# Kernel tuning notes

Hardware: AMD Instinct MI355X
Metric: run time of the kernel (lower is better)

## Reference

```python
import jax, jax.numpy as jnp
import numpy as np
import math

T, B, D, H, DH, DI, V, L = 1024, 4, 512, 8, 64, 2048, 256, 8
STAGES = (2, 4, 2)   # pre, shortened, post layer counts (model_config)
SF = 4               # fixed boundary every SF tokens
S = T // SF          # number of segments


def setup_inputs() -> dict:
    key = jax.random.key(0)
    ks = jax.random.split(key, 12)
    sd = 0.02
    data = jax.random.randint(ks[0], (T, B), 0, V, dtype=jnp.int32)
    t = jnp.arange(T)
    boundaries_gt = jnp.tile(((t % SF) == (SF - 1)).astype(jnp.int32)[:, None], (1, B))
    return {
        'data': data,
        'boundaries_gt': boundaries_gt,
        'word_emb': jax.random.normal(ks[1], (V, D)) * sd,
        'r_w_bias': jax.random.normal(ks[2], (H, DH)) * sd,
        'r_r_bias': jax.random.normal(ks[3], (H, DH)) * sd,
        'null_group': jax.random.normal(ks[4], (1, 1, D)),
        'down_ln_g': jnp.ones((D,), jnp.float32),
        'down_ln_b': jnp.zeros((D,), jnp.float32),
        'qkv_w': jax.random.normal(ks[5], (L, 3 * H * DH, D)) * sd,
        'rk_w': jax.random.normal(ks[6], (L, H * DH, D)) * sd,
        'o_w': jax.random.normal(ks[7], (L, D, H * DH)) * sd,
        'ln1_g': jnp.ones((L, D), jnp.float32),
        'ln1_b': jnp.zeros((L, D), jnp.float32),
        'ff_w1': jax.random.normal(ks[8], (L, DI, D)) * sd,
        'ff_b1': jnp.zeros((L, DI), jnp.float32),
        'ff_w2': jax.random.normal(ks[9], (L, D, DI)) * sd,
        'ff_b2': jnp.zeros((L, D), jnp.float32),
        'ln2_g': jnp.ones((L, D), jnp.float32),
        'ln2_b': jnp.zeros((L, D), jnp.float32),
        'final_w': jax.random.normal(ks[10], (V, D)) * sd,
        'final_b': jnp.zeros((V,), jnp.float32),
    }


def _ln(x, g, b):
    m = jnp.mean(x, -1, keepdims=True)
    v = jnp.mean((x - m) ** 2, -1, keepdims=True)
    return (x - m) * jax.lax.rsqrt(v + 1e-5) * g + b


def _pos_emb(qlen):
    # sinusoidal relative positions qlen-1 .. 0
    pos = jnp.arange(qlen - 1, -1, -1.0, dtype=jnp.float32)
    inv = 1.0 / (10000.0 ** (jnp.arange(0, D, 2, dtype=jnp.float32) / D))
    ang = pos[:, None] * inv[None, :]
    return jnp.concatenate([jnp.sin(ang), jnp.cos(ang)], -1)  # (qlen, D)


def _rel_shift(x):
    # x: (q, k, b, n) -- Transformer-XL relative shift
    q, k, b, n = x.shape
    x = jnp.pad(x, ((0, 0), (1, 0), (0, 0), (0, 0)))
    return x.reshape(k + 1, q, b, n)[1:].reshape(q, k, b, n)


def _stage(x, P, lo, hi, r_w_bias, r_r_bias):
    qkv_w, rk_w, o_w, ln1_g, ln1_b, w1, b1, w2, b2, ln2_g, ln2_b = P
    qlen, bsz, _ = x.shape
    r = _pos_emb(qlen)
    mask = jnp.triu(jnp.ones((qlen, qlen), bool), 1)  # causal
    scale = 1.0 / math.sqrt(DH)
    for i in range(lo, hi):
        h = x @ qkv_w[i].T                                  # (q,b,3HDh)
        qh, kh, vh = jnp.split(h, 3, axis=-1)
        qh = qh.reshape(qlen, bsz, H, DH)
        kh = kh.reshape(qlen, bsz, H, DH)
        vh = vh.reshape(qlen, bsz, H, DH)
        rk = (r @ rk_w[i].T).reshape(qlen, H, DH)
        AC = jnp.einsum('ibnd,jbnd->ijbn', qh + r_w_bias, kh)
        BD = _rel_shift(jnp.einsum('ibnd,jnd->ijbn', qh + r_r_bias, rk))
        score = jnp.where(mask[:, :, None, None], -1e30, (AC + BD) * scale)
        prob = jax.nn.softmax(score, axis=1)
        vec = jnp.einsum('ijbn,jbnd->ibnd', prob, vh).reshape(qlen, bsz, H * DH)
        x = _ln(x + vec @ o_w[i].T, ln1_g[i], ln1_b[i])      # post-LN
        ff = jax.nn.relu(x @ w1[i].T + b1[i]) @ w2[i].T + b2[i]
        x = _ln(x + ff, ln2_g[i], ln2_b[i])
    return x


def _downsample(bnd, hidden, null_group):
    # bnd: (B,T) float, hidden: (T,B,D). Mean-pool each segment, prepend null group.
    seg = jnp.cumsum(bnd, axis=1) - bnd                      # segment id per token
    ind = (seg[:, :, None] == jnp.arange(S, dtype=bnd.dtype)).astype(hidden.dtype)
    w = ind / (ind.sum(axis=1, keepdims=True) + 1e-9)        # (B,T,S)
    short = jnp.einsum('tbd,bts->sbd', hidden, w)
    null = jnp.tile(null_group, (1, hidden.shape[1], 1))
    return jnp.concatenate([null, short], axis=0)            # (S+1,B,D)


def _upsample(bnd, short):
    # token t copies segment cumsum(bnd)[t] (0 == null group)
    seg = jnp.cumsum(bnd, axis=1).astype(jnp.int32)          # (B,T) in [0,S]
    up = jnp.take_along_axis(short, seg.T[:, :, None], axis=0)  # (T,B,D)
    return up / (1.0 + 1e-9)                                 # matches 1/(1+eps) normalizer


def _forward(data, boundaries_gt, word_emb, r_w_bias, r_r_bias, null_group,
             down_ln_g, down_ln_b, qkv_w, rk_w, o_w, ln1_g, ln1_b,
             ff_w1, ff_b1, ff_w2, ff_b2, ln2_g, ln2_b, final_w, final_b):
    P = (qkv_w, rk_w, o_w, ln1_g, ln1_b, ff_w1, ff_b1, ff_w2, ff_b2, ln2_g, ln2_b)
    hidden = word_emb[data]                                  # (T,B,D)
    hidden = _stage(hidden, P, 0, STAGES[0], r_w_bias, r_r_bias)
    residual = hidden
    hard = boundaries_gt.astype(jnp.float32).T               # (B,T)
    short = _downsample(hard, hidden, null_group)
    short = _ln(short, down_ln_g, down_ln_b)
    short = _stage(short, P, STAGES[0], STAGES[0] + STAGES[1], r_w_bias, r_r_bias)
    hidden = _upsample(hard, short) + residual
    hidden = _stage(hidden, P, STAGES[0] + STAGES[1], L, r_w_bias, r_r_bias)
    return hidden @ final_w.T + final_b                      # logits (T,B,V)


def reference(data, boundaries_gt, word_emb, r_w_bias, r_r_bias, null_group,
              down_ln_g, down_ln_b, qkv_w, rk_w, o_w, ln1_g, ln1_b,
              ff_w1, ff_b1, ff_w2, ff_b2, ln2_g, ln2_b, final_w, final_b):
    return _forward(data, boundaries_gt, word_emb, r_w_bias, r_r_bias, null_group,
                    down_ln_g, down_ln_b, qkv_w, rk_w, o_w, ln1_g, ln1_b,
                    ff_w1, ff_b1, ff_w2, ff_b2, ln2_g, ln2_b, final_w, final_b)
```

## Files before the change

kernel.cpp:

```cpp
#include <hip/hip_runtime.h>
#include <math.h>

#define T_  1024
#define B_  4
#define D_  512
#define H_  8
#define DH_ 64
#define DI_ 2048
#define V_  256
#define L_  8
#define S_  256

typedef _Float16 f16;
typedef f16   f16x8 __attribute__((ext_vector_type(8)));
typedef float f32x4 __attribute__((ext_vector_type(4)));

__device__ __forceinline__ void gload16(const void* g, void* l) {
    __builtin_amdgcn_global_load_lds(
        (const __attribute__((address_space(1))) void*)g,
        (__attribute__((address_space(3))) void*)l, 16, 0, 0);
}

__constant__ int cIT[24] = {15,15,14,13,12,11,10, 9,  8, 7,14, 6,13, 5,12, 4,  8, 0, 9, 1,10, 2,11, 3};
__constant__ int cT0[24] = { 0, 8, 0, 0, 0, 0, 0, 0,  0, 0, 8, 0, 8, 0, 8, 0,  8, 0, 8, 0, 8, 0, 8, 0};
__constant__ int cT1[24] = { 8,16, 8, 8, 8, 8, 8, 8,  8, 8,15, 7,14, 6,13, 5,  9, 1,10, 2,11, 3,12, 4};
__constant__ int cIT2[8] = {4,4,3,3,2,2,1,0};
__constant__ int cT02[8] = {0,3,0,2,0,2,0,0};
__constant__ int cT12[8] = {3,5,2,4,2,3,2,1};

__global__ __launch_bounds__(256) void k_f2h(const float* __restrict__ s,
                                             f16* __restrict__ d, int n) {
    int i = (blockIdx.x * 256 + threadIdx.x) * 4;
    int stride = gridDim.x * 1024;
    for (; i < n; i += stride) {
        float4 v = *(const float4*)(s + i);
        d[i + 0] = (f16)v.x; d[i + 1] = (f16)v.y;
        d[i + 2] = (f16)v.z; d[i + 3] = (f16)v.w;
    }
}

__global__ __launch_bounds__(256) void k_embed(const int* __restrict__ data,
                                               const float* __restrict__ emb,
                                               float* __restrict__ x,
                                               f16* __restrict__ xh) {
    int idx = blockIdx.x * 256 + threadIdx.x;
    if (idx >= T_ * B_ * D_) return;
    int d  = idx & (D_ - 1);
    int tb = idx >> 9;
    float v = emb[(size_t)data[tb] * D_ + d];
    x[idx] = v; xh[idx] = (f16)v;
}

__global__ __launch_bounds__(256) void k_posemb(f16* __restrict__ r, int qlen) {
    int p = blockIdx.x;
    int k = threadIdx.x;
    float pos = (float)(qlen - 1 - p);
    float inv = powf(10000.f, -((float)k) / 256.f);
    float ang = pos * inv;
    r[(size_t)p * D_ + k]       = (f16)sinf(ang);
    r[(size_t)p * D_ + 256 + k] = (f16)cosf(ang);
}

template<int BM, int BN, int OUT16, int ACT>
__global__ __launch_bounds__(256) void k_gemm(const f16* __restrict__ X, int lda,
                                              const f16* __restrict__ W,
                                              const float* __restrict__ bias,
                                              void* __restrict__ Yv,
                                              int M, int N, int K) {
    __shared__ f16 As[BM * 64];
    __shared__ f16 Bs[BN * 64];
    const int tid = threadIdx.x, w = tid >> 6, lane = tid & 63;
    const int l16 = lane & 15, lg = lane >> 4;
    int nwg = gridDim.x * gridDim.y;
    int bid = blockIdx.y * gridDim.x + blockIdx.x;
    if ((nwg & 7) == 0) bid = (bid & 7) * (nwg >> 3) + (bid >> 3);
    const int bm = (bid % gridDim.x) * BM, bn = (bid / gridDim.x) * BN;
    const int lrow = lane >> 3, lcol = (lane & 7) * 8;
    constexpr int AI = (BM >= 32) ? BM / 32 : 1;
    constexpr int BI = BN / 32;
    constexpr int MI = (BN == 128) ? 4 : BM / 32;
    constexpr int NJ = 2;
    const int rbase = (BN == 128) ? 0 : (w >> 1) * (BM / 2);
    const int cbase = (BN == 128) ? w * 32 : (w & 1) * 32;
    const f32x4 z4 = {0.f, 0.f, 0.f, 0.f};
    f32x4 acc[MI][NJ];
    #pragma unroll
    for (int i = 0; i < MI; ++i)
        #pragma unroll
        for (int j = 0; j < NJ; ++j) acc[i][j] = z4;

    for (int k0 = 0; k0 < K; k0 += 64) {
        __syncthreads();
        #pragma unroll
        for (int u = 0; u < AI; ++u) {
            int rb = w * (BM / 4) + u * 8;
            gload16(X + (size_t)(bm + rb + lrow) * lda + k0 + lcol, &As[rb * 64]);
        }
        #pragma unroll
        for (int u = 0; u < BI; ++u) {
            int rb = w * (BN / 4) + u * 8;
            gload16(W + (size_t)(bn + rb + lrow) * K + k0 + lcol, &Bs[rb * 64]);
        }
        __syncthreads();
        __builtin_amdgcn_s_setprio(1);
        #pragma unroll
        for (int h = 0; h < 2; ++h) {
            f16x8 af[MI], bf[NJ];
            #pragma unroll
            for (int i = 0; i < MI; ++i)
                af[i] = *(const f16x8*)&As[(rbase + i * 16 + l16) * 64 + h * 32 + lg * 8];
            #pragma unroll
            for (int j = 0; j < NJ; ++j)
                bf[j] = *(const f16x8*)&Bs[(cbase + j * 16 + l16) * 64 + h * 32 + lg * 8];
            #pragma unroll
            for (int i = 0; i < MI; ++i)
                #pragma unroll
                for (int j = 0; j < NJ; ++j)
                    acc[i][j] = __builtin_amdgcn_mfma_f32_16x16x32_f16(af[i], bf[j], acc[i][j], 0, 0, 0);
        }
        __builtin_amdgcn_s_setprio(0);
    }
    #pragma unroll
    for (int i = 0; i < MI; ++i) {
        #pragma unroll
        for (int r = 0; r < 4; ++r) {
            int row = bm + rbase + i * 16 + lg * 4 + r;
            if (row >= M) continue;
            int colb = bn + cbase + l16;
            #pragma unroll
            for (int j = 0; j < NJ; ++j) {
                float v = acc[i][j][r];
                if (bias) v += bias[colb + j * 16];
                if (ACT) v = fmaxf(v, 0.f);
                if (OUT16) ((f16*)Yv)[(size_t)row * N + colb + j * 16] = (f16)v;
                else       ((float*)Yv)[(size_t)row * N + colb + j * 16] = v;
            }
        }
    }
}

__global__ __launch_bounds__(256) void k_ln(float* __restrict__ x,
                                            const f16* __restrict__ add,
                                            const float* __restrict__ g,
                                            const float* __restrict__ b,
                                            f16* __restrict__ xh, int rows) {
    int row = blockIdx.x * 4 + (threadIdx.x >> 6);
    if (row >= rows) return;
    int lane = threadIdx.x & 63;
    float* xr = x + (size_t)row * D_ + lane * 8;
    float v[8];
    {
        float4 a0 = *(const float4*)xr;
        float4 a1 = *(const float4*)(xr + 4);
        v[0] = a0.x; v[1] = a0.y; v[2] = a0.z; v[3] = a0.w;
        v[4] = a1.x; v[5] = a1.y; v[6] = a1.z; v[7] = a1.w;
    }
    if (add) {
        f16x8 a = *(const f16x8*)(add + (size_t)row * D_ + lane * 8);
        #pragma unroll
        for (int u = 0; u < 8; ++u) v[u] += (float)a[u];
    }
    float s = 0.f, sq = 0.f;
    #pragma unroll
    for (int u = 0; u < 8; ++u) { s += v[u]; sq += v[u] * v[u]; }
    #pragma unroll
    for (int off = 1; off < 64; off <<= 1) {
        s  += __shfl_xor(s,  off, 64);
        sq += __shfl_xor(sq, off, 64);
    }
    float mean = s * (1.f / (float)D_);
    float var  = sq * (1.f / (float)D_) - mean * mean;
    float rs   = rsqrtf(var + 1e-5f);
    const float* gp = g + lane * 8;
    const float* bp = b + lane * 8;
    float4 g0 = *(const float4*)gp, g1 = *(const float4*)(gp + 4);
    float4 b0 = *(const float4*)bp, b1 = *(const float4*)(bp + 4);
    float gg[8] = {g0.x, g0.y, g0.z, g0.w, g1.x, g1.y, g1.z, g1.w};
    float bb[8] = {b0.x, b0.y, b0.z, b0.w, b1.x, b1.y, b1.z, b1.w};
    float o[8];
    #pragma unroll
    for (int u = 0; u < 8; ++u) o[u] = (v[u] - mean) * rs * gg[u] + bb[u];
    *(float4*)xr       = make_float4(o[0], o[1], o[2], o[3]);
    *(float4*)(xr + 4) = make_float4(o[4], o[5], o[6], o[7]);
    f16x8 hv;
    #pragma unroll
    for (int u = 0; u < 8; ++u) hv[u] = (f16)o[u];
    *(f16x8*)(xh + (size_t)row * D_ + lane * 8) = hv;
}

__global__ __launch_bounds__(256) void k_downln(const float* __restrict__ x,
                                                const float* __restrict__ nullg,
                                                const float* __restrict__ g,
                                                const float* __restrict__ bi,
                                                float* __restrict__ xs,
                                                f16* __restrict__ xsh) {
    int row = blockIdx.x * 4 + (threadIdx.x >> 6);
    if (row >= (S_ + 1) * B_) return;
    int lane = threadIdx.x & 63;
    int s = row >> 2, b = row & 3;
    float v[8];
    if (s == 0) {
        const float* np = nullg + lane * 8;
        float4 a0 = *(const float4*)np, a1 = *(const float4*)(np + 4);
        v[0] = a0.x; v[1] = a0.y; v[2] = a0.z; v[3] = a0.w;
        v[4] = a1.x; v[5] = a1.y; v[6] = a1.z; v[7] = a1.w;
    } else {
        int t0 = (s - 1) * 4;
        #pragma unroll
        for (int u = 0; u < 8; ++u) v[u] = 0.f;
        #pragma unroll
        for (int k = 0; k < 4; ++k) {
            const float* xp = x + ((size_t)(t0 + k) * B_ + b) * D_ + lane * 8;
            float4 a0 = *(const float4*)xp, a1 = *(const float4*)(xp + 4);
            v[0] += a0.x; v[1] += a0.y; v[2] += a0.z; v[3] += a0.w;
            v[4] += a1.x; v[5] += a1.y; v[6] += a1.z; v[7] += a1.w;
        }
        #pragma unroll
        for (int u = 0; u < 8; ++u) v[u] *= 0.25f;
    }
    float sm = 0.f, sq = 0.f;
    #pragma unroll
    for (int u = 0; u < 8; ++u) { sm += v[u]; sq += v[u] * v[u]; }
    #pragma unroll
    for (int off = 1; off < 64; off <<= 1) {
        sm += __shfl_xor(sm, off, 64);
        sq += __shfl_xor(sq, off, 64);
    }
    float mean = sm * (1.f / (float)D_);
    float var  = sq * (1.f / (float)D_) - mean * mean;
    float rs   = rsqrtf(var + 1e-5f);
    float o[8];
    #pragma unroll
    for (int u = 0; u < 8; ++u)
        o[u] = (v[u] - mean) * rs * g[lane * 8 + u] + bi[lane * 8 + u];
    float* xp = xs + (size_t)row * D_ + lane * 8;
    *(float4*)xp       = make_float4(o[0], o[1], o[2], o[3]);
    *(float4*)(xp + 4) = make_float4(o[4], o[5], o[6], o[7]);
    f16x8 hv;
    #pragma unroll
    for (int u = 0; u < 8; ++u) hv[u] = (f16)o[u];
    *(f16x8*)(xsh + (size_t)row * D_ + lane * 8) = hv;
}

__global__ __launch_bounds__(256) void k_up(float* __restrict__ x,
                                            const float* __restrict__ xs,
                                            f16* __restrict__ xh) {
    int idx = blockIdx.x * 256 + threadIdx.x;
    if (idx >= T_ * B_ * D_) return;
    int d  = idx & (D_ - 1);
    int tb = idx >> 9;
    int t = tb >> 2, b = tb & 3;
    int seg = (t + 1) >> 2;
    float v = x[idx] + xs[((size_t)seg * B_ + b) * D_ + d];
    x[idx] = v; xh[idx] = (f16)v;
}

__global__ __launch_bounds__(256) void k_attn(f16* __restrict__ qkv,
                                              const f16* __restrict__ rkb,
                                              int ldr,
                                              const float* __restrict__ rwb,
                                              const float* __restrict__ rrb,
                                              int Q, float* __restrict__ part) {
    __shared__ f16 RKs[192 * 64];
    __shared__ f16 Ks[64 * 64];
    __shared__ f16 Vt[64 * 72];
    __shared__ f16 Pl[4][16 * 72];
    f16* Qw = RKs;
    f16* Qr = RKs + 4096;

    int it, t0, t1, b, n;
    bool partial;
    int idxp;
    {
        int p = blockIdx.y * gridDim.x + blockIdx.x;
        int xcd = p & 7, qq = p >> 3;
        b = xcd >> 1;
        n = (xcd & 1) * 4 + (qq & 3);
        int slot = qq >> 2;
        if (Q == 1024) {
            it = cIT[slot]; t0 = cT0[slot]; t1 = cT1[slot];
            partial = (it >= 8);
            idxp = (b * 8 + n) * 8 + (it - 8);
        } else {
            it = cIT2[slot]; t0 = cT02[slot]; t1 = cT12[slot];
            partial = (it >= 2);
            idxp = (b * 8 + n) * 3 + (it - 2);
        }
    }
    const int i0 = it * 64;
    const int tid = threadIdx.x, w = tid >> 6, lane = tid & 63;
    const int l16 = lane & 15, lg = lane >> 4;
    const int xsw = (l16 & 7) << 3;
    const int gr8 = lane >> 3;
    const int gsl = ((lane & 7) ^ gr8) * 8;
    const int vjj = tid >> 2, vdb = (tid & 3) * 16;
    const int wb = 48 - w * 16;
    const f32x4 z4 = {0.f, 0.f, 0.f, 0.f};

    {
        int row = tid >> 2, dq = (tid & 3) * 16;
        const f16* qp = qkv + ((size_t)(i0 + row) * B_ + b) * 1536 + n * 64 + dq;
        f16x8 q0 = *(const f16x8*)qp, q1 = *(const f16x8*)(qp + 8);
        int rsw = (row & 7) << 3;
        #pragma unroll
        for (int u = 0; u < 8; ++u) {
            float qa = (float)q0[u], qb2 = (float)q1[u];
            Qw[row * 64 + ((dq + u) ^ rsw)]     = (f16)(qa + rwb[n * 64 + dq + u]);
            Qw[row * 64 + ((dq + 8 + u) ^ rsw)] = (f16)(qb2 + rwb[n * 64 + dq + 8 + u]);
            Qr[row * 64 + ((dq + u) ^ rsw)]     = (f16)(qa + rrb[n * 64 + dq + u]);
            Qr[row * 64 + ((dq + 8 + u) ^ rsw)] = (f16)(qb2 + rrb[n * 64 + dq + 8 + u]);
        }
    }
    __syncthreads();
    f16x8 aqw[2], aqr[2];
    #pragma unroll
    for (int h = 0; h < 2; ++h) {
        aqw[h] = *(const f16x8*)&Qw[(w * 16 + l16) * 64 + ((h * 32 + lg * 8) ^ xsw)];
        aqr[h] = *(const f16x8*)&Qr[(w * 16 + l16) * 64 + ((h * 32 + lg * 8) ^ xsw)];
    }
    __syncthreads();

    const long long pb = (long long)Q - 64 - i0;
    #pragma unroll
    for (int u = 0; u < 4; ++u) {
        int rb = w * 32 + u * 8;
        long long p = pb + t0 * 64 + rb + gr8;
        gload16(rkb + p * ldr + n * 64 + gsl, &RKs[rb * 64]);
    }
    #pragma unroll
    for (int u = 0; u < 2; ++u) {
        int rb = w * 16 + u * 8;
        gload16(qkv + ((size_t)(t0 * 64 + rb + gr8) * B_ + b) * 1536 + 512 + n * 64 + gsl,
                &Ks[rb * 64]);
    }
    f16x8 vr0, vr1;
    {
        const f16* vp = qkv + ((size_t)(t0 * 64 + vjj) * B_ + b) * 1536 + 1024 + n * 64 + vdb;
        vr0 = *(const f16x8*)vp; vr1 = *(const f16x8*)(vp + 8);
    }

    f32x4 acc[4]; acc[0] = z4; acc[1] = z4; acc[2] = z4; acc[3] = z4;
    float psum[4] = {0.f, 0.f, 0.f, 0.f};
    int base = 0;

    for (int t = t0; t < t1; ++t) {
        const int j0 = t * 64;
        __syncthreads();
        #pragma unroll
        for (int u = 0; u < 8; ++u) {
            Vt[(vdb + u) * 72 + (vjj ^ ((u & 7) << 3))]     = vr0[u];
            Vt[(vdb + 8 + u) * 72 + (vjj ^ ((u & 7) << 3))] = vr1[u];
        }
        if (t + 1 < t1) {
            int sb = base + 128; if (sb >= 192) sb -= 192;
            #pragma unroll
            for (int u = 0; u < 2; ++u) {
                int rb = w * 16 + u * 8;
                long long p = pb + j0 + 128 + rb + gr8;
                gload16(rkb + p * ldr + n * 64 + gsl, &RKs[(sb + rb) * 64]);
            }
        }
        f32x4 s1[4]; s1[0] = z4; s1[1] = z4; s1[2] = z4; s1[3] = z4;
        __builtin_amdgcn_s_setprio(1);
        #pragma unroll
        for (int f = 0; f < 4; ++f)
            #pragma unroll
            for (int h = 0; h < 2; ++h) {
                f16x8 bv = *(const f16x8*)&Ks[(f * 16 + l16) * 64 + ((h * 32 + lg * 8) ^ xsw)];
                s1[f] = __builtin_amdgcn_mfma_f32_16x16x32_f16(aqw[h], bv, s1[f], 0, 0, 0);
            }
        __builtin_amdgcn_s_setprio(0);
        if (t + 1 < t1) {
            const f16* vp = qkv + ((size_t)(j0 + 64 + vjj) * B_ + b) * 1536 + 1024 + n * 64 + vdb;
            vr0 = *(const f16x8*)vp; vr1 = *(const f16x8*)(vp + 8);
        }
        f32x4 s2[5]; s2[0] = z4; s2[1] = z4; s2[2] = z4; s2[3] = z4; s2[4] = z4;
        __builtin_amdgcn_s_setprio(1);
        #pragma unroll
        for (int f = 0; f < 5; ++f) {
            int slot = base + wb + f * 16 + l16; if (slot >= 192) slot -= 192;
            #pragma unroll
            for (int h = 0; h < 2; ++h) {
                f16x8 bv = *(const f16x8*)&RKs[slot * 64 + ((h * 32 + lg * 8) ^ xsw)];
                s2[f] = __builtin_amdgcn_mfma_f32_16x16x32_f16(aqr[h], bv, s2[f], 0, 0, 0);
            }
        }
        __builtin_amdgcn_s_setprio(0);
        #pragma unroll
        for (int r = 0; r < 4; ++r) {
            const int q = lg * 4 + r;
            const int iq = i0 + w * 16 + q;
            const int src = (lane & 48) | ((l16 + 15 - q) & 15);
            float g0 = __shfl(s2[0][r], src, 64);
            float g1 = __shfl(s2[1][r], src, 64);
            float g2 = __shfl(s2[2][r], src, 64);
            float g3 = __shfl(s2[3][r], src, 64);
            float g4 = __shfl(s2[4][r], src, 64);
            const bool hi = l16 > q;
            float sv[4];
            sv[0] = (s1[0][r] + (hi ? g1 : g0)) * 0.125f;
            sv[1] = (s1[1][r] + (hi ? g2 : g1)) * 0.125f;
            sv[2] = (s1[2][r] + (hi ? g3 : g2)) * 0.125f;
            sv[3] = (s1[3][r] + (hi ? g4 : g3)) * 0.125f;
            #pragma unroll
            for (int h = 0; h < 4; ++h) {
                int j = j0 + h * 16 + l16;
                if (j > iq || j >= Q) sv[h] = -1e30f;
            }
            float p0 = __expf(sv[0]), p1 = __expf(sv[1]);
            float p2 = __expf(sv[2]), p3 = __expf(sv[3]);
            psum[r] += (p0 + p1) + (p2 + p3);
            Pl[w][q * 72 + l16]      = (f16)p0;
            Pl[w][q * 72 + 16 + l16] = (f16)p1;
            Pl[w][q * 72 + 32 + l16] = (f16)p2;
            Pl[w][q * 72 + 48 + l16] = (f16)p3;
        }
        __syncthreads();
        f16x8 pa0 = *(const f16x8*)&Pl[w][l16 * 72 + lg * 8];
        f16x8 pa1 = *(const f16x8*)&Pl[w][l16 * 72 + 32 + lg * 8];
        __builtin_amdgcn_s_setprio(1);
        #pragma unroll
        for (int f = 0; f < 4; ++f) {
            f16x8 bv0 = *(const f16x8*)&Vt[(f * 16 + l16) * 72 + ((lg * 8) ^ xsw)];
            acc[f] = __builtin_amdgcn_mfma_f32_16x16x32_f16(pa0, bv0, acc[f], 0, 0, 0);
            f16x8 bv1 = *(const f16x8*)&Vt[(f * 16 + l16) * 72 + ((32 + lg * 8) ^ xsw)];
            acc[f] = __builtin_amdgcn_mfma_f32_16x16x32_f16(pa1, bv1, acc[f], 0, 0, 0);
        }
        __builtin_amdgcn_s_setprio(0);
        if (t + 1 < t1) {
            #pragma unroll
            for (int u = 0; u < 2; ++u) {
                int rb = w * 16 + u * 8;
                gload16(qkv + ((size_t)(j0 + 64 + rb + gr8) * B_ + b) * 1536 + 512 + n * 64 + gsl,
                        &Ks[rb * 64]);
            }
        }
        base += 64; if (base >= 192) base -= 192;
    }
    if (partial) {
        float* Pp = part + (size_t)idxp * 8320 + (t0 ? 4160 : 0);
        #pragma unroll
        for (int r = 0; r < 4; ++r) {
            float ps = psum[r];
            ps += __shfl_xor(ps, 1, 64);
            ps += __shfl_xor(ps, 2, 64);
            ps += __shfl_xor(ps, 4, 64);
            ps += __shfl_xor(ps, 8, 64);
            int row = w * 16 + lg * 4 + r;
            #pragma unroll
            for (int f = 0; f < 4; ++f)
                Pp[row * 64 + f * 16 + l16] = acc[f][r];
            if (l16 == 0) Pp[4096 + row] = ps;
        }
    } else {
        #pragma unroll
        for (int r = 0; r < 4; ++r) {
            float ps = psum[r];
            ps += __shfl_xor(ps, 1, 64);
            ps += __shfl_xor(ps, 2, 64);
            ps += __shfl_xor(ps, 4, 64);
            ps += __shfl_xor(ps, 8, 64);
            int i = i0 + w * 16 + lg * 4 + r;
            if (i < Q) {
                float inv = 1.f / ps;
                f16* op = qkv + ((size_t)i * B_ + b) * 1536 + n * 64;
                #pragma unroll
                for (int f = 0; f < 4; ++f)
                    op[f * 16 + l16] = (f16)(acc[f][r] * inv);
            }
        }
    }
}

__global__ __launch_bounds__(256) void k_comb(const float* __restrict__ part,
                                              f16* __restrict__ qkv,
                                              int nm, int itbase, int Q) {
    int idxp = blockIdx.x;
    int m = idxp % nm;
    int bn = idxp / nm;
    int b = bn >> 3, n = bn & 7;
    int i0 = (m + itbase) * 64;
    int row = threadIdx.x >> 2, dp = (threadIdx.x & 3) * 16;
    if (i0 + row >= Q) return;
    const float* A  = part + (size_t)idxp * 8320;
    const float* Bp = A + 4160;
    float inv = 1.f / (A[4096 + row] + Bp[4096 + row]);
    f16* op = qkv + ((size_t)(i0 + row) * B_ + b) * 1536 + n * 64 + dp;
    #pragma unroll
    for (int k = 0; k < 16; k += 4) {
        float4 a  = *(const float4*)(A  + row * 64 + dp + k);
        float4 bb = *(const float4*)(Bp + row * 64 + dp + k);
        op[k + 0] = (f16)((a.x + bb.x) * inv);
        op[k + 1] = (f16)((a.y + bb.y) * inv);
        op[k + 2] = (f16)((a.z + bb.z) * inv);
        op[k + 3] = (f16)((a.w + bb.w) * inv);
    }
}

extern "C" void kernel_launch(void* const* d_in, const int* in_sizes, int n_in,
                              void* d_out, int out_size, void* d_ws, size_t ws_size,
                              hipStream_t stream) {
    const int*   data     = (const int*)  d_in[0];
    const float* word_emb = (const float*)d_in[2];
    const float* rwb      = (const float*)d_in[3];
    const float* rrb      = (const float*)d_in[4];
    const float* nullg    = (const float*)d_in[5];
    const float* dg       = (const float*)d_in[6];
    const float* db       = (const float*)d_in[7];
    const float* qkv_w    = (const float*)d_in[8];
    const float* rk_w     = (const float*)d_in[9];
    const float* o_w      = (const float*)d_in[10];
    const float* ln1g     = (const float*)d_in[11];
    const float* ln1b     = (const float*)d_in[12];
    const float* w1       = (const float*)d_in[13];
    const float* b1       = (const float*)d_in[14];
    const float* w2       = (const float*)d_in[15];
    const float* b2       = (const float*)d_in[16];
    const float* ln2g     = (const float*)d_in[17];
    const float* ln2b     = (const float*)d_in[18];
    const float* fw       = (const float*)d_in[19];
    const float* fb       = (const float*)d_in[20];
    float* out = (float*)d_out;
    float* ws  = (float*)d_ws;

    float* x    = ws;
    float* tmp  = x + 2097152;
    float* xs   = tmp + 2097152;
    f16* xh     = (f16*)(xs + 589824);
    f16* xsh    = xh + 2097152;
    f16* r1h    = xsh + 589824;
    f16* r2h    = r1h + 524288;
    f16* rkall  = r2h + 163840;
    f16* bigh   = rkall + 2623488;
    f16* qkv_wh = bigh + 8388608;
    f16* rk_wh  = qkv_wh + 6291456;
    f16* o_wh   = rk_wh + 2097152;
    f16* w1h    = o_wh + 2097152;
    f16* w2h    = w1h + 8388608;
    f16* fwh    = w2h + 8388608;
    f16* tmph   = (f16*)tmp;

    auto conv = [&](const float* s, f16* d, int n) {
        int blocks = min(2048, (n + 1023) / 1024);
        k_f2h<<<blocks, 256, 0, stream>>>(s, d, n);
    };
    conv(qkv_w, qkv_wh, L_ * 1536 * 512);
    conv(rk_w,  rk_wh,  L_ * 512 * 512);
    conv(o_w,   o_wh,   L_ * 512 * 512);
    conv(w1,    w1h,    L_ * 2048 * 512);
    conv(w2,    w2h,    L_ * 512 * 2048);
    conv(fw,    fwh,    256 * 512);

    auto gemm = [&](const f16* Xp, int lda, const f16* Wp, const float* bp,
                    void* Yp, int M, int N, int K, int out16, int act) {
        int b64_128 = (N % 128 == 0) ? ((M + 63) / 64) * (N / 128) : 0;
        if (b64_128 >= 768) {
            dim3 g((M + 63) / 64, N / 128);
            if (out16) {
                if (act) k_gemm<64, 128, 1, 1><<<g, 256, 0, stream>>>(Xp, lda, Wp, bp, Yp, M, N, K);
                else     k_gemm<64, 128, 1, 0><<<g, 256, 0, stream>>>(Xp, lda, Wp, bp, Yp, M, N, K);
            } else      k_gemm<64, 128, 0, 0><<<g, 256, 0, stream>>>(Xp, lda, Wp, bp, Yp, M, N, K);
            return;
        }
        int b64_64 = ((M + 63) / 64) * (N / 64);
        if (b64_64 >= 768) {
            dim3 g((M + 63) / 64, N / 64);
            if (out16) {
                if (act) k_gemm<64, 64, 1, 1><<<g, 256, 0, stream>>>(Xp, lda, Wp, bp, Yp, M, N, K);
                else     k_gemm<64, 64, 1, 0><<<g, 256, 0, stream>>>(Xp, lda, Wp, bp, Yp, M, N, K);
            } else      k_gemm<64, 64, 0, 0><<<g, 256, 0, stream>>>(Xp, lda, Wp, bp, Yp, M, N, K);
            return;
        }
        dim3 g((M + 31) / 32, N / 64);
        if (out16) {
            if (act) k_gemm<32, 64, 1, 1><<<g, 256, 0, stream>>>(Xp, lda, Wp, bp, Yp, M, N, K);
            else     k_gemm<32, 64, 1, 0><<<g, 256, 0, stream>>>(Xp, lda, Wp, bp, Yp, M, N, K);
        } else      k_gemm<32, 64, 0, 0><<<g, 256, 0, stream>>>(Xp, lda, Wp, bp, Yp, M, N, K);
    };

    k_embed<<<8192, 256, 0, stream>>>(data, word_emb, x, xh);
    k_posemb<<<1024, 256, 0, stream>>>(r1h, 1024);
    k_posemb<<<257, 256, 0, stream>>>(r2h, 257);

    gemm(r1h, 512, rk_wh,                nullptr, rkall,           1024, 1024, 512, 1, 0);
    gemm(r1h, 512, rk_wh + 6 * 262144,   nullptr, rkall + 1048576, 1024, 1024, 512, 1, 0);
    gemm(r2h, 512, rk_wh + 2 * 262144,   nullptr, rkall + 2097152,  257, 2048, 512, 1, 0);

    auto stage = [&](float* xb, f16* xbh, int Q, int lo, int hi) {
        const int M = Q * B_;
        dim3 gA = (Q == 1024) ? dim3(24, 32) : dim3(8, 32);
        dim3 gL((M + 3) / 4);
        for (int i = lo; i < hi; ++i) {
            const f16* rkp; int ldr;
            if (i < 2)       { rkp = rkall + i * 512;                 ldr = 1024; }
            else if (i >= 6) { rkp = rkall + 1048576 + (i - 6) * 512; ldr = 1024; }
            else             { rkp = rkall + 2097152 + (i - 2) * 512; ldr = 2048; }
            gemm(xbh, 512, qkv_wh + (size_t)i * 786432, nullptr, bigh, M, 1536, 512, 1, 0);
            k_attn<<<gA, 256, 0, stream>>>(bigh, rkp, ldr, rwb, rrb, Q, tmp);
            if (Q == 1024) k_comb<<<256, 256, 0, stream>>>(tmp, bigh, 8, 8, 1024);
            else           k_comb<<<96, 256, 0, stream>>>(tmp, bigh, 3, 2, 257);
            gemm(bigh, 1536, o_wh + (size_t)i * 262144, nullptr, tmph, M, 512, 512, 1, 0);
            k_ln<<<gL, 256, 0, stream>>>(xb, tmph, ln1g + (size_t)i * 512, ln1b + (size_t)i * 512, xbh, M);
            gemm(xbh, 512, w1h + (size_t)i * 1048576, b1 + (size_t)i * 2048, bigh, M, 2048, 512, 1, 1);
            gemm(bigh, 2048, w2h + (size_t)i * 1048576, b2 + (size_t)i * 512, tmph, M, 512, 2048, 1, 0);
            k_ln<<<gL, 256, 0, stream>>>(xb, tmph, ln2g + (size_t)i * 512, ln2b + (size_t)i * 512, xbh, M);
        }
    };

    stage(x, xh, 1024, 0, 2);
    k_downln<<<257, 256, 0, stream>>>(x, nullg, dg, db, xs, xsh);
    stage(xs, xsh, S_ + 1, 2, 6);
    k_up<<<8192, 256, 0, stream>>>(x, xs, xh);
    stage(x, xh, 1024, 6, 8);
    gemm(xh, 512, fwh, fb, out, T_ * B_, V_, 512, 0, 0);
}
```

Baseline: 851.9 us.

## Double-buffer GEMM LDS tiles and fold softmax scale into Q with exp2

The GEMM kernel now uses two LDS buffers, so the global-to-LDS load of the next K tile is issued before the MFMAs on the current tile, with one barrier per iteration instead of two. This is meant to overlap memory latency with compute, at the cost of doubling LDS use per block, which may lower occupancy. The attention kernel pre-multiplies Q by 0.125*log2(e) when staging it and replaces the score scale plus __expf with exp2f, removing per-element multiplies. The AI constant also drops its BM<32 guard.

Measured after the change: 865.8 us. Within noise of the previous version (+1.6%).

```diff
diff --git a/kernel.cpp b/kernel.cpp
--- a/kernel.cpp
+++ b/kernel.cpp
@@ -14,6 +14,8 @@
 typedef _Float16 f16;
 typedef f16   f16x8 __attribute__((ext_vector_type(8)));
 typedef float f32x4 __attribute__((ext_vector_type(4)));
+
+#define SC_ 0.18033688f
 
 __device__ __forceinline__ void gload16(const void* g, void* l) {
     __builtin_amdgcn_global_load_lds(
@@ -67,8 +69,8 @@
                                               const float* __restrict__ bias,
                                               void* __restrict__ Yv,
                                               int M, int N, int K) {
-    __shared__ f16 As[BM * 64];
-    __shared__ f16 Bs[BN * 64];
+    __shared__ f16 As[2][BM * 64];
+    __shared__ f16 Bs[2][BN * 64];
     const int tid = threadIdx.x, w = tid >> 6, lane = tid & 63;
     const int l16 = lane & 15, lg = lane >> 4;
     int nwg = gridDim.x * gridDim.y;
@@ -76,7 +78,7 @@
     if ((nwg & 7) == 0) bid = (bid & 7) * (nwg >> 3) + (bid >> 3);
     const int bm = (bid % gridDim.x) * BM, bn = (bid / gridDim.x) * BN;
     const int lrow = lane >> 3, lcol = (lane & 7) * 8;
-    constexpr int AI = (BM >= 32) ? BM / 32 : 1;
+    constexpr int AI = BM / 32;
     constexpr int BI = BN / 32;
     constexpr int MI = (BN == 128) ? 4 : BM / 32;
     constexpr int NJ = 2;
@@ -89,29 +91,34 @@
         #pragma unroll
         for (int j = 0; j < NJ; ++j) acc[i][j] = z4;
 
-    for (int k0 = 0; k0 < K; k0 += 64) {
-        __syncthreads();
+    auto stage = [&](int buf, int k0) {
         #pragma unroll
         for (int u = 0; u < AI; ++u) {
             int rb = w * (BM / 4) + u * 8;
-            gload16(X + (size_t)(bm + rb + lrow) * lda + k0 + lcol, &As[rb * 64]);
+            gload16(X + (size_t)(bm + rb + lrow) * lda + k0 + lcol, &As[buf][rb * 64]);
         }
         #pragma unroll
         for (int u = 0; u < BI; ++u) {
             int rb = w * (BN / 4) + u * 8;
-            gload16(W + (size_t)(bn + rb + lrow) * K + k0 + lcol, &Bs[rb * 64]);
-        }
-        __syncthreads();
+            gload16(W + (size_t)(bn + rb + lrow) * K + k0 + lcol, &Bs[buf][rb * 64]);
+        }
+    };
+
+    stage(0, 0);
+    __syncthreads();
+    int cur = 0;
+    for (int k0 = 0; k0 < K; k0 += 64) {
+        if (k0 + 64 < K) stage(cur ^ 1, k0 + 64);
         __builtin_amdgcn_s_setprio(1);
         #pragma unroll
         for (int h = 0; h < 2; ++h) {
             f16x8 af[MI], bf[NJ];
             #pragma unroll
             for (int i = 0; i < MI; ++i)
-                af[i] = *(const f16x8*)&As[(rbase + i * 16 + l16) * 64 + h * 32 + lg * 8];
+                af[i] = *(const f16x8*)&As[cur][(rbase + i * 16 + l16) * 64 + h * 32 + lg * 8];
             #pragma unroll
             for (int j = 0; j < NJ; ++j)
-                bf[j] = *(const f16x8*)&Bs[(cbase + j * 16 + l16) * 64 + h * 32 + lg * 8];
+                bf[j] = *(const f16x8*)&Bs[cur][(cbase + j * 16 + l16) * 64 + h * 32 + lg * 8];
             #pragma unroll
             for (int i = 0; i < MI; ++i)
                 #pragma unroll
@@ -119,6 +126,8 @@
                     acc[i][j] = __builtin_amdgcn_mfma_f32_16x16x32_f16(af[i], bf[j], acc[i][j], 0, 0, 0);
         }
         __builtin_amdgcn_s_setprio(0);
+        __syncthreads();
+        cur ^= 1;
     }
     #pragma unroll
     for (int i = 0; i < MI; ++i) {
@@ -305,10 +314,10 @@
         #pragma unroll
         for (int u = 0; u < 8; ++u) {
             float qa = (float)q0[u], qb2 = (float)q1[u];
-            Qw[row * 64 + ((dq + u) ^ rsw)]     = (f16)(qa + rwb[n * 64 + dq + u]);
-            Qw[row * 64 + ((dq + 8 + u) ^ rsw)] = (f16)(qb2 + rwb[n * 64 + dq + 8 + u]);
-            Qr[row * 64 + ((dq + u) ^ rsw)]     = (f16)(qa + rrb[n * 64 + dq + u]);
-            Qr[row * 64 + ((dq + 8 + u) ^ rsw)] = (f16)(qb2 + rrb[n * 64 + dq + 8 + u]);
+            Qw[row * 64 + ((dq + u) ^ rsw)]     = (f16)((qa + rwb[n * 64 + dq + u]) * SC_);
+            Qw[row * 64 + ((dq + 8 + u) ^ rsw)] = (f16)((qb2 + rwb[n * 64 + dq + 8 + u]) * SC_);
+            Qr[row * 64 + ((dq + u) ^ rsw)]     = (f16)((qa + rrb[n * 64 + dq + u]) * SC_);
+            Qr[row * 64 + ((dq + 8 + u) ^ rsw)] = (f16)((qb2 + rrb[n * 64 + dq + 8 + u]) * SC_);
         }
     }
     __syncthreads();
@@ -398,17 +407,17 @@
             float g4 = __shfl(s2[4][r], src, 64);
             const bool hi = l16 > q;
             float sv[4];
-            sv[0] = (s1[0][r] + (hi ? g1 : g0)) * 0.125f;
-            sv[1] = (s1[1][r] + (hi ? g2 : g1)) * 0.125f;
-            sv[2] = (s1[2][r] + (hi ? g3 : g2)) * 0.125f;
-            sv[3] = (s1[3][r] + (hi ? g4 : g3)) * 0.125f;
+            sv[0] = s1[0][r] + (hi ? g1 : g0);
+            sv[1] = s1[1][r] + (hi ? g2 : g1);
+            sv[2] = s1[2][r] + (hi ? g3 : g2);
+            sv[3] = s1[3][r] + (hi ? g4 : g3);
             #pragma unroll
             for (int h = 0; h < 4; ++h) {
                 int j = j0 + h * 16 + l16;
                 if (j > iq || j >= Q) sv[h] = -1e30f;
             }
-            float p0 = __expf(sv[0]), p1 = __expf(sv[1]);
-            float p2 = __expf(sv[2]), p3 = __expf(sv[3]);
+            float p0 = exp2f(sv[0]), p1 = exp2f(sv[1]);
+            float p2 = exp2f(sv[2]), p3 = exp2f(sv[3]);
             psum[r] += (p0 + p1) + (p2 + p3);
             Pl[w][q * 72 + l16]      = (f16)p0;
             Pl[w][q * 72 + 16 + l16] = (f16)p1;
```
